# Kernel tuning notes

Measured on AMD Instinct MI355X. Metric: run time of the kernel, lower is better.

Reference implementation:

```python
import jax, jax.numpy as jnp
import numpy as np

HIDDEN = 2048
NUM_HEADS = 16
NUM_KV_HEADS = 8
HEAD_DIM = 128
EPS = 1e-6
ROPE_THETA = 10000.0
Q_SIZE = NUM_HEADS * HEAD_DIM
KV_SIZE = NUM_KV_HEADS * HEAD_DIM


def setup_inputs() -> dict:
    key = jax.random.key(0)
    k1, k2, k3 = jax.random.split(key, 3)
    B, S = 2, 2048
    positions = jnp.broadcast_to(jnp.arange(S, dtype=jnp.int32), (B, S))
    hidden_states = jax.random.normal(k1, (B, S, HIDDEN), dtype=jnp.float32)
    w_qkv = jax.random.normal(k2, (Q_SIZE + 2 * KV_SIZE, HIDDEN), dtype=jnp.float32) * (HIDDEN ** -0.5)
    w_o = jax.random.normal(k3, (HIDDEN, Q_SIZE), dtype=jnp.float32) * (Q_SIZE ** -0.5)
    q_norm_w = jnp.ones((HEAD_DIM,), dtype=jnp.float32)
    k_norm_w = jnp.ones((HEAD_DIM,), dtype=jnp.float32)
    return {"positions": positions, "hidden_states": hidden_states,
            "w_qkv": w_qkv, "w_o": w_o, "q_norm_w": q_norm_w, "k_norm_w": k_norm_w}


def _rms_norm(x, w):
    # x: [..., HEAD_DIM]
    var = jnp.mean(x * x, axis=-1, keepdims=True)
    return x * jax.lax.rsqrt(var + EPS) * w


def _rope(x, cos, sin):
    # x: [B, S, H, D]; cos/sin: [B, S, 1, D/2] (neox style: rotate half)
    x1, x2 = jnp.split(x, 2, axis=-1)
    return jnp.concatenate([x1 * cos - x2 * sin, x2 * cos + x1 * sin], axis=-1)


def reference(positions, hidden_states, w_qkv, w_o, q_norm_w, k_norm_w):
    B, S, _ = hidden_states.shape
    qkv = jnp.einsum("bsh,oh->bso", hidden_states, w_qkv)
    q, k, v = jnp.split(qkv, [Q_SIZE, Q_SIZE + KV_SIZE], axis=-1)
    q = q.reshape(B, S, NUM_HEADS, HEAD_DIM)
    k = k.reshape(B, S, NUM_KV_HEADS, HEAD_DIM)
    v = v.reshape(B, S, NUM_KV_HEADS, HEAD_DIM)

    # per-head RMSNorm on q and k (Qwen3 qk-norm)
    q = _rms_norm(q, q_norm_w)
    k = _rms_norm(k, k_norm_w)

    # RoPE (neox style)
    inv_freq = 1.0 / (ROPE_THETA ** (jnp.arange(0, HEAD_DIM, 2, dtype=jnp.float32) / HEAD_DIM))
    angles = positions.astype(jnp.float32)[..., None] * inv_freq  # [B, S, D/2]
    cos = jnp.cos(angles)[:, :, None, :]
    sin = jnp.sin(angles)[:, :, None, :]
    q = _rope(q, cos, sin)
    k = _rope(k, cos, sin)

    # GQA: expand kv heads to match q heads
    rep = NUM_HEADS // NUM_KV_HEADS
    k = jnp.repeat(k, rep, axis=2)  # [B, S, H, D]
    v = jnp.repeat(v, rep, axis=2)

    scale = HEAD_DIM ** -0.5
    scores = jnp.einsum("bqhd,bkhd->bhqk", q, k) * scale
    causal = jnp.tril(jnp.ones((S, S), dtype=bool))
    scores = jnp.where(causal, scores, jnp.finfo(scores.dtype).min)
    probs = jax.nn.softmax(scores, axis=-1)
    attn = jnp.einsum("bhqk,bkhd->bqhd", probs, v).reshape(B, S, Q_SIZE)
    return jnp.einsum("bso,ho->bsh", attn, w_o)
```

## Files before the change

### kernel.cpp

```cpp
#include <hip/hip_runtime.h>
#include <hip/hip_bf16.h>
#include <cstdint>
#include <cstddef>

#define HIDDEN 2048
#define NHEADS 16
#define NKV    8
#define HD     128
#define QS     (NHEADS*HD)
#define KVS    (NKV*HD)
#define OC     (QS + 2*KVS)
#define BB     2
#define SS     2048
#define ROWS   (BB*SS)

typedef __bf16 bf16;
typedef __bf16 bf16x8 __attribute__((ext_vector_type(8)));
typedef __bf16 bf16x4 __attribute__((ext_vector_type(4)));
typedef float  f32x4  __attribute__((ext_vector_type(4)));
typedef float  f32x2  __attribute__((ext_vector_type(2)));
typedef float  f32x16 __attribute__((ext_vector_type(16)));
typedef int    i32x4  __attribute__((ext_vector_type(4)));

__device__ __forceinline__ float fexp2(float x) {
#if __has_builtin(__builtin_amdgcn_exp2f)
  return __builtin_amdgcn_exp2f(x);
#else
  return __expf(x * 0.6931471805599453f);
#endif
}


__global__ __launch_bounds__(256) void k_cvtb(const float* __restrict__ src,
                                              bf16* __restrict__ dst, int nchunks) {
  int G = blockIdx.x * blockDim.x + threadIdx.x;
  int stride = gridDim.x * blockDim.x;
  for (; G < nchunks; G += stride) {
    int c = G & 1023, tile = G >> 10;
    int P = tile >> 5, kt = tile & 31;
    int hg = c & 1, l31 = (c >> 1) & 31, s = (c >> 6) & 3, rg = c >> 8;
    int row = P * 128 + rg * 32 + l31;
    int k = kt * 64 + s * 16 + hg * 8;
    const f32x4* sp = (const f32x4*)(src + (size_t)row * 2048 + k);
    f32x4 a = sp[0], b2 = sp[1];
    bf16x8 o;
    o[0]=(bf16)a[0]; o[1]=(bf16)a[1]; o[2]=(bf16)a[2]; o[3]=(bf16)a[3];
    o[4]=(bf16)b2[0]; o[5]=(bf16)b2[1]; o[6]=(bf16)b2[2]; o[7]=(bf16)b2[3];
    *(bf16x8*)(dst + (size_t)G * 8) = o;
  }
}

__global__ __launch_bounds__(256) void k_cvtb2(const float* __restrict__ s0, bf16* __restrict__ d0, int n0,
                                               const float* __restrict__ s1, bf16* __restrict__ d1, int n1) {
  int G = blockIdx.x * blockDim.x + threadIdx.x;
  int stride = gridDim.x * blockDim.x;
  int total = n0 + n1;
  for (; G < total; G += stride) {
    const float* src; bf16* dst; int g;
    if (G < n0) { src = s0; dst = d0; g = G; }
    else        { src = s1; dst = d1; g = G - n0; }
    int c = g & 1023, tile = g >> 10;
    int P = tile >> 6, kt = tile & 63;
    int hg = c & 1, l31 = (c >> 1) & 31, s = (c >> 6) & 1, rg = c >> 7;
    int row = P * 256 + rg * 32 + l31;
    int k = kt * 32 + s * 16 + hg * 8;
    const f32x4* sp = (const f32x4*)(src + (size_t)row * 2048 + k);
    f32x4 a = sp[0], b2 = sp[1];
    bf16x8 o;
    o[0]=(bf16)a[0]; o[1]=(bf16)a[1]; o[2]=(bf16)a[2]; o[3]=(bf16)a[3];
    o[4]=(bf16)b2[0]; o[5]=(bf16)b2[1]; o[6]=(bf16)b2[2]; o[7]=(bf16)b2[3];
    *(bf16x8*)(dst + (size_t)g * 8) = o;
  }
}

__global__ __launch_bounds__(256) void k_table(float* __restrict__ tbl) {
  int t = blockIdx.x * blockDim.x + threadIdx.x;
  int pos = t >> 6, i = t & 63;
  float freq = powf(10000.0f, -(float)i / 64.0f);
  float ang = (float)pos * freq;
  float sv, cv;
  sincosf(ang, &sv, &cv);
  f32x2 v; v[0] = cv; v[1] = sv;
  ((f32x2*)tbl)[t] = v;
}

__device__ __forceinline__ void gll16(const void* g, void* l) {
  __builtin_amdgcn_global_load_lds((const __attribute__((address_space(1))) void*)g,
                                   (__attribute__((address_space(3))) void*)l, 16, 0, 0);
}

__global__ __launch_bounds__(512) void k_gemm1(const bf16* __restrict__ A,
                                               const bf16* __restrict__ Bw,
                                               bf16* __restrict__ C,
                                               int M, int N, int K) {
  const int tid = threadIdx.x;
  const int lane = tid & 63;
  const int w = tid >> 6;
  const int lin = blockIdx.x + gridDim.x * blockIdx.y;
  const int cpx = (gridDim.x * gridDim.y) >> 3;
  const int swz = (lin & 7) * cpx + (lin >> 3);
  const int bx = swz % gridDim.x, by = swz / gridDim.x;
  const int m0 = by * 256, n0 = bx * 256;
  __shared__ bf16 Abuf[4][8192];
  __shared__ bf16 Bbuf[4][8192];
  f32x16 acc[4][2] = {};
  const int l31 = lane & 31, hg = lane >> 5;
  const int rgwA = (w >> 2) * 4;
  const int rgwB = (w & 3) * 2;
  const int KT = K >> 5;
  const size_t baseA = ((size_t)(m0 >> 8) * KT) << 13;
  const size_t baseB = ((size_t)(n0 >> 8) * KT) << 13;
  #pragma unroll
  for (int p = 0; p < 3; ++p) {
    #pragma unroll
    for (int i = 0; i < 2; ++i) {
      int c = tid + i * 512;
      gll16(A + baseA + ((size_t)p << 13) + (size_t)c * 8, Abuf[p] + (size_t)(c & ~63) * 8);
      gll16(Bw + baseB + ((size_t)p << 13) + (size_t)c * 8, Bbuf[p] + (size_t)(c & ~63) * 8);
    }
  }
  for (int t = 0; t < KT; ++t) {
    const int rem = KT - 1 - t;
    if (rem >= 2)      asm volatile("s_waitcnt vmcnt(8)" ::: "memory");
    else if (rem == 1) asm volatile("s_waitcnt vmcnt(4)" ::: "memory");
    else               asm volatile("s_waitcnt vmcnt(0)" ::: "memory");
    __syncthreads();
    if (t + 3 < KT) {
      const int nt3 = t + 3, nb = nt3 & 3;
      #pragma unroll
      for (int i = 0; i < 2; ++i) {
        int c = tid + i * 512;
        gll16(A + baseA + ((size_t)nt3 << 13) + (size_t)c * 8, Abuf[nb] + (size_t)(c & ~63) * 8);
        gll16(Bw + baseB + ((size_t)nt3 << 13) + (size_t)c * 8, Bbuf[nb] + (size_t)(c & ~63) * 8);
      }
    }
    const char* Ab = (const char*)Abuf[t & 3];
    const char* Bb = (const char*)Bbuf[t & 3];
    __builtin_amdgcn_s_setprio(1);
    #pragma unroll
    for (int s = 0; s < 2; ++s) {
      bf16x8 af[4], bfv[2];
      #pragma unroll
      for (int i = 0; i < 4; ++i)
        af[i] = *(const bf16x8*)(Ab + (((rgwA + i) * 2 + s) * 1024 + l31 * 32 + hg * 16));
      #pragma unroll
      for (int j = 0; j < 2; ++j)
        bfv[j] = *(const bf16x8*)(Bb + (((rgwB + j) * 2 + s) * 1024 + l31 * 32 + hg * 16));
      #pragma unroll
      for (int i = 0; i < 4; ++i)
        #pragma unroll
        for (int j = 0; j < 2; ++j)
          acc[i][j] = __builtin_amdgcn_mfma_f32_32x32x16_bf16(af[i], bfv[j], acc[i][j], 0, 0, 0);
    }
    __builtin_amdgcn_s_setprio(0);
  }
  #pragma unroll
  for (int i = 0; i < 4; ++i)
    #pragma unroll
    for (int j = 0; j < 2; ++j) {
      int col = n0 + (w & 3) * 64 + j * 32 + l31;
      #pragma unroll
      for (int reg = 0; reg < 16; ++reg) {
        int row = m0 + (w >> 2) * 128 + i * 32 + 4 * hg + (reg & 3) + 8 * (reg >> 2);
        C[(size_t)row * N + col] = (bf16)acc[i][j][reg];
      }
    }
}

template <typename OT>
__global__ __launch_bounds__(256) void k_gemm(const bf16* __restrict__ A,
                                              const bf16* __restrict__ Bw,
                                              OT* __restrict__ C,
                                              int M, int N, int K) {
  const int tid = threadIdx.x;
  const int lane = tid & 63;
  const int w = tid >> 6;
  const int lin = blockIdx.x + gridDim.x * blockIdx.y;
  const int cpx = (gridDim.x * gridDim.y) >> 3;
  const int swz = (lin & 7) * cpx + (lin >> 3);
  const int bx = swz % gridDim.x, by = swz / gridDim.x;
  const int m0 = by * 128, n0 = bx * 128;
  __shared__ bf16 As[128 * 64];
  __shared__ bf16 Bs[128 * 64];
  f32x16 acc[2][2] = {};
  const int wm = (w >> 1) * 64, wn = (w & 1) * 64;
  const int l31 = lane & 31, hg = lane >> 5;
  const int rgA = (w >> 1) * 2;
  const int rgB = (w & 1) * 2;
  const int KT = K >> 6;
  const int kt0 = ((lin >> 8) & 3) * (KT >> 2);
  for (int it = 0; it < KT; ++it) {
    int kt = kt0 + it; if (kt >= KT) kt -= KT;
    __syncthreads();
    const size_t tA = ((size_t)((m0 >> 7) * KT + kt)) << 13;
    const size_t tB = ((size_t)((n0 >> 7) * KT + kt)) << 13;
    #pragma unroll
    for (int i = 0; i < 4; ++i) {
      int c = tid + i * 256;
      gll16(A + tA + (size_t)c * 8, As + (size_t)(c & ~63) * 8);
      gll16(Bw + tB + (size_t)c * 8, Bs + (size_t)(c & ~63) * 8);
    }
    asm volatile("s_waitcnt vmcnt(0)" ::: "memory");
    __syncthreads();
    bf16x8 af[2][4], bfv[2][4];
    #pragma unroll
    for (int i = 0; i < 2; ++i)
      #pragma unroll
      for (int s = 0; s < 4; ++s)
        af[i][s] = *(const bf16x8*)((char*)As + (((rgA + i) * 4 + s) * 1024 + l31 * 32 + hg * 16));
    #pragma unroll
    for (int j = 0; j < 2; ++j)
      #pragma unroll
      for (int s = 0; s < 4; ++s)
        bfv[j][s] = *(const bf16x8*)((char*)Bs + (((rgB + j) * 4 + s) * 1024 + l31 * 32 + hg * 16));
    #pragma unroll
    for (int i = 0; i < 2; ++i)
      #pragma unroll
      for (int j = 0; j < 2; ++j)
        #pragma unroll
        for (int s = 0; s < 4; ++s)
          acc[i][j] = __builtin_amdgcn_mfma_f32_32x32x16_bf16(af[i][s], bfv[j][s], acc[i][j], 0, 0, 0);
  }
  #pragma unroll
  for (int i = 0; i < 2; ++i)
    #pragma unroll
    for (int j = 0; j < 2; ++j) {
      int col = n0 + wn + j * 32 + l31;
      #pragma unroll
      for (int reg = 0; reg < 16; ++reg) {
        int row = m0 + wm + i * 32 + 4 * hg + (reg & 3) + 8 * (reg >> 2);
        C[(size_t)row * N + col] = (OT)acc[i][j][reg];
      }
    }
}

__global__ __launch_bounds__(256) void k_ropenorm(const bf16* __restrict__ qkv,
                                                  bf16* __restrict__ qb, bf16* __restrict__ kb,
                                                  const float* __restrict__ tbl,
                                                  const int* __restrict__ pos,
                                                  const float* __restrict__ qw,
                                                  const float* __restrict__ kw) {
  int gw = blockIdx.x * 4 + (threadIdx.x >> 6);
  int lane = threadIdx.x & 63;
  int h = gw % 24;
  int rem = gw / 24;
  int s = rem & (SS - 1);
  int b = rem >> 11;
  size_t row = (size_t)b * SS + s;
  int col0 = (h < 16) ? h * HD : QS + (h - 16) * HD;
  unsigned u = *(const unsigned*)(qkv + row * OC + col0 + lane * 2);
  float x0 = __uint_as_float((u & 0xffffu) << 16);
  float x1 = __uint_as_float(u & 0xffff0000u);
  float ssq = x0 * x0 + x1 * x1;
  for (int m = 1; m < 64; m <<= 1) ssq += __shfl_xor(ssq, m, 64);
  float r = rsqrtf(ssq * (1.0f / 128.0f) + 1e-6f);
  const float* wv = (h < 16) ? qw : kw;
  float y0 = x0 * r * wv[lane * 2], y1 = x1 * r * wv[lane * 2 + 1];
  float p0 = __shfl_xor(y0, 32, 64), p1 = __shfl_xor(y1, 32, 64);
  int p = pos[row];
  f32x4 cs = *(const f32x4*)(tbl + (size_t)p * 128 + (lane & 31) * 4);
  float o0, o1;
  if (lane < 32) { o0 = y0 * cs[0] - p0 * cs[1]; o1 = y1 * cs[2] - p1 * cs[3]; }
  else           { o0 = y0 * cs[0] + p0 * cs[1]; o1 = y1 * cs[2] + p1 * cs[3]; }
  bf16* dst; size_t drow;
  if (h < 16) {
    const float scl2 = 0.12753102f;
    o0 *= scl2; o1 *= scl2;
    dst = qb; drow = ((size_t)b * NHEADS + h) * SS + s;
  } else {
    dst = kb; drow = ((size_t)b * NKV + (h - 16)) * SS + s;
  }
  bf16 v0 = (bf16)o0, v1 = (bf16)o1;
  unsigned short q0, q1;
  __builtin_memcpy(&q0, &v0, 2); __builtin_memcpy(&q1, &v1, 2);
  *(unsigned*)(dst + drow * HD + lane * 2) = (unsigned)q0 | ((unsigned)q1 << 16);
}

__global__ __launch_bounds__(256) void k_vt(const bf16* __restrict__ qkv,
                                            bf16* __restrict__ vT) {
  __shared__ bf16 T[64 * 136];
  int tid = threadIdx.x;
  int st = blockIdx.x, kv = blockIdx.y, b = blockIdx.z;
  int s0 = st * 64;
  for (int i = 0; i < 4; ++i) {
    int c = tid + i * 256;
    int sl = c >> 4, dc = c & 15;
    i32x4 v = *(const i32x4*)(qkv + (size_t)(b * SS + s0 + sl) * OC + QS + KVS + kv * HD + dc * 8);
    *(i32x4*)(T + sl * 136 + dc * 8) = v;
  }
  __syncthreads();
  for (int i = 0; i < 4; ++i) {
    int c = tid + i * 256;
    int d = c >> 3, sg = c & 7;
    bf16x8 o;
    for (int j = 0; j < 8; ++j) o[j] = T[(sg * 8 + j) * 136 + d];
    *(bf16x8*)(vT + ((size_t)(b * NKV + kv) * HD + d) * SS + s0 + sg * 8) = o;
  }
}

__global__ __launch_bounds__(256) void k_attn9(const bf16* __restrict__ qb,
                                               const bf16* __restrict__ kb,
                                               const bf16* __restrict__ vT,
                                               bf16* __restrict__ out) {
  __shared__ bf16 Kl[64 * 128];
  __shared__ bf16 Vl[128 * 64];
  __shared__ bf16 Pl[4][16 * 64];
  const int tid = threadIdx.x, lane = tid & 63, w = tid >> 6;
  const int L = blockIdx.x + 32 * (blockIdx.y + 16 * blockIdx.z);
  const int r8 = L & 7;
  const int c4 = (L >> 3) & 3;
  const int i32_ = L >> 5;
  const int g = r8 * 4 + c4;
  const int h = g >> 1, b = g & 1;
  const int a_ = i32_ & 7, m_ = i32_ >> 3;
  const int qt = (m_ == 0) ? a_ : (m_ == 1) ? (15 - a_) : (m_ == 2) ? (16 + a_) : (31 - a_);
  const int kvh = h >> 1;
  const int lr = lane & 15, lg = lane >> 4;
  const int qbase = qt * 64 + w * 16;
  const float NEG = -3.0e38f;
  bf16x8 qf[4];
  {
    const bf16* qrow = qb + ((size_t)(b * NHEADS + h) * SS + qbase + lr) * HD;
    #pragma unroll
    for (int ks = 0; ks < 4; ++ks) qf[ks] = *(const bf16x8*)(qrow + ks * 32 + lg * 8);
  }
  f32x4 acc[8] = {};
  float m_r = NEG, l_r = 0.0f;
  const bf16* Kg = kb + (size_t)(b * NKV + kvh) * SS * HD;
  const bf16* Vg = vT + (size_t)(b * NKV + kvh) * HD * SS;
  for (int t = 0; t <= qt; ++t) {
    const int kv0 = t * 64;
    __syncthreads();
    #pragma unroll
    for (int i = 0; i < 4; ++i) {
      int c = tid + i * 256;
      int r_ = c >> 4;
      int ch = (c & 15) ^ (r_ & 7);
      gll16(Kg + (size_t)(kv0 + r_) * HD + ch * 8, Kl + (size_t)(c & ~63) * 8);
    }
    #pragma unroll
    for (int i = 0; i < 4; ++i) {
      int c = tid + i * 256;
      int d = c >> 3;
      int ch = (c & 7) ^ (d & 7);
      gll16(Vg + (size_t)d * SS + kv0 + ch * 8, Vl + (size_t)(c & ~63) * 8);
    }
    asm volatile("s_waitcnt vmcnt(0)" ::: "memory");
    __syncthreads();
    f32x4 sf[4];
    __builtin_amdgcn_s_setprio(1);
    #pragma unroll
    for (int mt = 0; mt < 4; ++mt) {
      f32x4 a2 = {0.f, 0.f, 0.f, 0.f};
      const int rrow = mt * 16 + lr;
      #pragma unroll
      for (int ks = 0; ks < 4; ++ks) {
        bf16x8 kf = *(const bf16x8*)((char*)Kl + ((rrow * 256 + ks * 64 + lg * 16) ^ ((rrow & 7) << 4)));
        a2 = __builtin_amdgcn_mfma_f32_16x16x32_bf16(kf, qf[ks], a2, 0, 0, 0);
      }
      sf[mt] = a2;
    }
    __builtin_amdgcn_s_setprio(0);
    const int qg = qbase + lr;
    float pm = NEG;
    if (t == qt) {
      #pragma unroll
      for (int mt = 0; mt < 4; ++mt)
        #pragma unroll
        for (int r = 0; r < 4; ++r) {
          int kvg = kv0 + mt * 16 + lg * 4 + r;
          float v = sf[mt][r];
          if (kvg > qg) v = NEG;
          sf[mt][r] = v;
          pm = fmaxf(pm, v);
        }
    } else {
      #pragma unroll
      for (int mt = 0; mt < 4; ++mt)
        #pragma unroll
        for (int r = 0; r < 4; ++r) pm = fmaxf(pm, sf[mt][r]);
    }
    pm = fmaxf(pm, __shfl_xor(pm, 16, 64));
    pm = fmaxf(pm, __shfl_xor(pm, 32, 64));
    if (!__all(pm <= m_r + 11.5415603f)) {
      const float mn = fmaxf(m_r, pm);
      const float scale = fexp2(m_r - mn);
      float sr[4];
      #pragma unroll
      for (int r = 0; r < 4; ++r) sr[r] = __shfl(scale, lg * 4 + r, 64);
      #pragma unroll
      for (int nt = 0; nt < 8; ++nt)
        #pragma unroll
        for (int r = 0; r < 4; ++r) acc[nt][r] *= sr[r];
      l_r *= scale;
      m_r = mn;
    }
    float ts = 0.f;
    #pragma unroll
    for (int mt = 0; mt < 4; ++mt)
      #pragma unroll
      for (int r = 0; r < 4; ++r) {
        float pv = fexp2(sf[mt][r] - m_r);
        sf[mt][r] = pv;
        ts += pv;
      }
    ts += __shfl_xor(ts, 16, 64);
    ts += __shfl_xor(ts, 32, 64);
    l_r += ts;
    #pragma unroll
    for (int mt = 0; mt < 4; ++mt) {
      bf16x4 pk;
      #pragma unroll
      for (int r = 0; r < 4; ++r) pk[r] = (bf16)sf[mt][r];
      *(bf16x4*)((char*)&Pl[w][0] + ((lr * 128 + mt * 32 + lg * 8) ^ ((lr & 7) << 4))) = pk;
    }
    __builtin_amdgcn_s_setprio(1);
    #pragma unroll
    for (int kk = 0; kk < 2; ++kk) {
      bf16x8 pa = *(const bf16x8*)((char*)&Pl[w][0] + ((lr * 128 + kk * 64 + lg * 16) ^ ((lr & 7) << 4)));
      #pragma unroll
      for (int nt = 0; nt < 8; ++nt) {
        const int d = nt * 16 + lr;
        bf16x8 vbf = *(const bf16x8*)((char*)Vl + ((d * 128 + kk * 64 + lg * 16) ^ ((d & 7) << 4)));
        acc[nt] = __builtin_amdgcn_mfma_f32_16x16x32_bf16(pa, vbf, acc[nt], 0, 0, 0);
      }
    }
    __builtin_amdgcn_s_setprio(0);
  }
  const float inv = 1.0f / l_r;
  float ir[4];
  #pragma unroll
  for (int r = 0; r < 4; ++r) ir[r] = __shfl(inv, lg * 4 + r, 64);
  const int hgE = (lr >> 3) & 1, eE = lr & 7;
  #pragma unroll
  for (int nt = 0; nt < 8; ++nt) {
    const int ktE = h * 2 + (nt >> 2);
    const int sE = nt & 3;
    #pragma unroll
    for (int r = 0; r < 4; ++r) {
      int rowi = b * SS + qbase + lg * 4 + r;
      int P = rowi >> 7, rr = rowi & 127;
      int rg = rr >> 5, l31r = rr & 31;
      int cE = ((rg * 4 + sE) * 32 + l31r) * 2 + hgE;
      size_t addr = (((size_t)(P * 32 + ktE)) << 13) + (size_t)cE * 8 + eE;
      out[addr] = (bf16)(acc[nt][r] * ir[r]);
    }
  }
}

extern "C" void kernel_launch(void* const* d_in, const int* in_sizes, int n_in,
                              void* d_out, int out_size, void* d_ws, size_t ws_size,
                              hipStream_t stream) {
  const int*   pos  = (const int*)d_in[0];
  const float* hid  = (const float*)d_in[1];
  const float* wqkv = (const float*)d_in[2];
  const float* wo   = (const float*)d_in[3];
  const float* qw   = (const float*)d_in[4];
  const float* kw   = (const float*)d_in[5];
  char* ws = (char*)d_ws;
  bf16* hid_bf  = (bf16*)(ws + 0);
  bf16* attn_o  = hid_bf;
  bf16* wqkv_bf = (bf16*)(ws + 16777216);
  bf16* q_buf   = wqkv_bf;
  bf16* k_buf   = (bf16*)(ws + 33554432);
  bf16* wo_bf   = k_buf;
  bf16* qkv     = (bf16*)(ws + 41943040);
  bf16* vT      = (bf16*)(ws + 75497472);
  float* tbl    = (float*)(ws + 83886080);

  k_cvtb2<<<dim3(2048), dim3(256), 0, stream>>>(
      hid, hid_bf, ROWS * HIDDEN / 8,
      wqkv, wqkv_bf, OC * HIDDEN / 8);
  k_table<<<dim3(512), dim3(256), 0, stream>>>(tbl);
  k_gemm1<<<dim3(OC / 256, ROWS / 256), dim3(512), 0, stream>>>(
      hid_bf, wqkv_bf, qkv, ROWS, OC, HIDDEN);
  k_ropenorm<<<dim3(ROWS * 24 / 4), dim3(256), 0, stream>>>(
      qkv, q_buf, k_buf, tbl, pos, qw, kw);
  k_vt<<<dim3(SS / 64, NKV, BB), dim3(256), 0, stream>>>(qkv, vT);
  k_attn9<<<dim3(SS / 64, NHEADS, BB), dim3(256), 0, stream>>>(
      q_buf, k_buf, vT, attn_o);
  k_cvtb<<<dim3(2048), dim3(256), 0, stream>>>(wo, wo_bf, HIDDEN * QS / 8);
  k_gemm<float><<<dim3(HIDDEN / 128, ROWS / 128), dim3(256), 0, stream>>>(
      attn_o, wo_bf, (float*)d_out, ROWS, HIDDEN, QS);
}
```

Baseline: 254.3 us.

## Double-buffer LDS tiles in GEMM and attention kernels to overlap loads

Both the GEMM and the flash-attention kernel now keep two LDS buffers and issue global-to-LDS loads for the next K/V (or A/B) tile before computing on the current one. A partial vmcnt wait lets the current tile's loads finish while the next tile's stay in flight. This hides global memory latency behind MFMA work. The cost is doubled LDS use, which may lower occupancy. The GEMM also drops its rotated k-start offset and raises wave priority around the MFMA section.

```diff
diff --git a/kernel.cpp b/kernel.cpp
--- a/kernel.cpp
+++ b/kernel.cpp
@@ -180,39 +180,54 @@
   const int swz = (lin & 7) * cpx + (lin >> 3);
   const int bx = swz % gridDim.x, by = swz / gridDim.x;
   const int m0 = by * 128, n0 = bx * 128;
-  __shared__ bf16 As[128 * 64];
-  __shared__ bf16 Bs[128 * 64];
+  __shared__ bf16 As[2][128 * 64];
+  __shared__ bf16 Bs[2][128 * 64];
   f32x16 acc[2][2] = {};
-  const int wm = (w >> 1) * 64, wn = (w & 1) * 64;
+  const int wn = (w & 1) * 64;
+  const int wm = (w >> 1) * 64;
   const int l31 = lane & 31, hg = lane >> 5;
   const int rgA = (w >> 1) * 2;
   const int rgB = (w & 1) * 2;
   const int KT = K >> 6;
-  const int kt0 = ((lin >> 8) & 3) * (KT >> 2);
+  const size_t baseA = ((size_t)(m0 >> 7) * KT) << 13;
+  const size_t baseB = ((size_t)(n0 >> 7) * KT) << 13;
+  #pragma unroll
+  for (int i = 0; i < 4; ++i) {
+    int c = tid + i * 256;
+    gll16(A + baseA + (size_t)c * 8, As[0] + (size_t)(c & ~63) * 8);
+    gll16(Bw + baseB + (size_t)c * 8, Bs[0] + (size_t)(c & ~63) * 8);
+  }
   for (int it = 0; it < KT; ++it) {
-    int kt = kt0 + it; if (kt >= KT) kt -= KT;
     __syncthreads();
-    const size_t tA = ((size_t)((m0 >> 7) * KT + kt)) << 13;
-    const size_t tB = ((size_t)((n0 >> 7) * KT + kt)) << 13;
-    #pragma unroll
-    for (int i = 0; i < 4; ++i) {
-      int c = tid + i * 256;
-      gll16(A + tA + (size_t)c * 8, As + (size_t)(c & ~63) * 8);
-      gll16(Bw + tB + (size_t)c * 8, Bs + (size_t)(c & ~63) * 8);
-    }
-    asm volatile("s_waitcnt vmcnt(0)" ::: "memory");
+    if (it + 1 < KT) {
+      const int nb = (it + 1) & 1;
+      const size_t oA = baseA + ((size_t)(it + 1) << 13);
+      const size_t oB = baseB + ((size_t)(it + 1) << 13);
+      #pragma unroll
+      for (int i = 0; i < 4; ++i) {
+        int c = tid + i * 256;
+        gll16(A + oA + (size_t)c * 8, As[nb] + (size_t)(c & ~63) * 8);
+        gll16(Bw + oB + (size_t)c * 8, Bs[nb] + (size_t)(c & ~63) * 8);
+      }
+      asm volatile("s_waitcnt vmcnt(8)" ::: "memory");
+    } else {
+      asm volatile("s_waitcnt vmcnt(0)" ::: "memory");
+    }
     __syncthreads();
+    const char* Ab = (const char*)As[it & 1];
+    const char* Bb = (const char*)Bs[it & 1];
+    __builtin_amdgcn_s_setprio(1);
     bf16x8 af[2][4], bfv[2][4];
     #pragma unroll
     for (int i = 0; i < 2; ++i)
       #pragma unroll
       for (int s = 0; s < 4; ++s)
-        af[i][s] = *(const bf16x8*)((char*)As + (((rgA + i) * 4 + s) * 1024 + l31 * 32 + hg * 16));
+        af[i][s] = *(const bf16x8*)(Ab + (((rgA + i) * 4 + s) * 1024 + l31 * 32 + hg * 16));
     #pragma unroll
     for (int j = 0; j < 2; ++j)
       #pragma unroll
       for (int s = 0; s < 4; ++s)
-        bfv[j][s] = *(const bf16x8*)((char*)Bs + (((rgB + j) * 4 + s) * 1024 + l31 * 32 + hg * 16));
+        bfv[j][s] = *(const bf16x8*)(Bb + (((rgB + j) * 4 + s) * 1024 + l31 * 32 + hg * 16));
     #pragma unroll
     for (int i = 0; i < 2; ++i)
       #pragma unroll
@@ -220,6 +235,7 @@
         #pragma unroll
         for (int s = 0; s < 4; ++s)
           acc[i][j] = __builtin_amdgcn_mfma_f32_32x32x16_bf16(af[i][s], bfv[j][s], acc[i][j], 0, 0, 0);
+    __builtin_amdgcn_s_setprio(0);
   }
   #pragma unroll
   for (int i = 0; i < 2; ++i)
@@ -302,8 +318,8 @@
                                                const bf16* __restrict__ kb,
                                                const bf16* __restrict__ vT,
                                                bf16* __restrict__ out) {
-  __shared__ bf16 Kl[64 * 128];
-  __shared__ bf16 Vl[128 * 64];
+  __shared__ bf16 Kl[2][64 * 128];
+  __shared__ bf16 Vl[2][128 * 64];
   __shared__ bf16 Pl[4][16 * 64];
   const int tid = threadIdx.x, lane = tid & 63, w = tid >> 6;
   const int L = blockIdx.x + 32 * (blockIdx.y + 16 * blockIdx.z);
@@ -328,25 +344,47 @@
   float m_r = NEG, l_r = 0.0f;
   const bf16* Kg = kb + (size_t)(b * NKV + kvh) * SS * HD;
   const bf16* Vg = vT + (size_t)(b * NKV + kvh) * HD * SS;
+  #pragma unroll
+  for (int i = 0; i < 4; ++i) {
+    int c = tid + i * 256;
+    int r_ = c >> 4;
+    int ch = (c & 15) ^ (r_ & 7);
+    gll16(Kg + (size_t)r_ * HD + ch * 8, Kl[0] + (size_t)(c & ~63) * 8);
+  }
+  #pragma unroll
+  for (int i = 0; i < 4; ++i) {
+    int c = tid + i * 256;
+    int d = c >> 3;
+    int ch = (c & 7) ^ (d & 7);
+    gll16(Vg + (size_t)d * SS + ch * 8, Vl[0] + (size_t)(c & ~63) * 8);
+  }
   for (int t = 0; t <= qt; ++t) {
+    __syncthreads();
+    if (t + 1 <= qt) {
+      const int nb = (t + 1) & 1;
+      const int nkv0 = (t + 1) * 64;
+      #pragma unroll
+      for (int i = 0; i < 4; ++i) {
+        int c = tid + i * 256;
+        int r_ = c >> 4;
+        int ch = (c & 15) ^ (r_ & 7);
+        gll16(Kg + (size_t)(nkv0 + r_) * HD + ch * 8, Kl[nb] + (size_t)(c & ~63) * 8);
+      }
+      #pragma unroll
+      for (int i = 0; i < 4; ++i) {
+        int c = tid + i * 256;
+        int d = c >> 3;
+        int ch = (c & 7) ^ (d & 7);
+        gll16(Vg + (size_t)d * SS + nkv0 + ch * 8, Vl[nb] + (size_t)(c & ~63) * 8);
+      }
+      asm volatile("s_waitcnt vmcnt(8)" ::: "memory");
+    } else {
+      asm volatile("s_waitcnt vmcnt(0)" ::: "memory");
+    }
+    __syncthreads();
+    const char* Kc = (const char*)Kl[t & 1];
+    const char* Vc = (const char*)Vl[t & 1];
     const int kv0 = t * 64;
-    __syncthreads();
-    #pragma unroll
-    for (int i = 0; i < 4; ++i) {
-      int c = tid + i * 256;
-      int r_ = c >> 4;
-      int ch = (c & 15) ^ (r_ & 7);
-      gll16(Kg + (size_t)(kv0 + r_) * HD + ch * 8, Kl + (size_t)(c & ~63) * 8);
-    }
-    #pragma unroll
-    for (int i = 0; i < 4; ++i) {
-      int c = tid + i * 256;
-      int d = c >> 3;
-      int ch = (c & 7) ^ (d & 7);
-      gll16(Vg + (size_t)d * SS + kv0 + ch * 8, Vl + (size_t)(c & ~63) * 8);
-    }
-    asm volatile("s_waitcnt vmcnt(0)" ::: "memory");
-    __syncthreads();
     f32x4 sf[4];
     __builtin_amdgcn_s_setprio(1);
     #pragma unroll
@@ -355,7 +393,7 @@
       const int rrow = mt * 16 + lr;
       #pragma unroll
       for (int ks = 0; ks < 4; ++ks) {
-        bf16x8 kf = *(const bf16x8*)((char*)Kl + ((rrow * 256 + ks * 64 + lg * 16) ^ ((rrow & 7) << 4)));
+        bf16x8 kf = *(const bf16x8*)(Kc + ((rrow * 256 + ks * 64 + lg * 16) ^ ((rrow & 7) << 4)));
         a2 = __builtin_amdgcn_mfma_f32_16x16x32_bf16(kf, qf[ks], a2, 0, 0, 0);
       }
       sf[mt] = a2;
@@ -421,7 +459,7 @@
       #pragma unroll
       for (int nt = 0; nt < 8; ++nt) {
         const int d = nt * 16 + lr;
-        bf16x8 vbf = *(const bf16x8*)((char*)Vl + ((d * 128 + kk * 64 + lg * 16) ^ ((d & 7) << 4)));
+        bf16x8 vbf = *(const bf16x8*)(Vc + ((d * 128 + kk * 64 + lg * 16) ^ ((d & 7) << 4)));
         acc[nt] = __builtin_amdgcn_mfma_f32_16x16x32_bf16(pa, vbf, acc[nt], 0, 0, 0);
       }
     }
```

Result: no change. 257.7 us (+1.4%).
